# Optimization experiments

Measured on AMD Instinct MI355X. Metric: run time of the kernel, lower is better.

Reference implementation:

```python
import jax, jax.numpy as jnp
import numpy as np

B, L, D_MODEL, H = 2, 2048, 1024, 16
HD = D_MODEL // H  # head dim = 64


def setup_inputs() -> dict:
    key = jax.random.key(0)
    ks = jax.random.split(key, 11)
    s = 1.0 / np.sqrt(D_MODEL)
    inp = {
        "Q": jax.random.normal(ks[0], (B, L, D_MODEL), jnp.float32),
        "K": jax.random.normal(ks[1], (B, L, D_MODEL), jnp.float32),
        "V": jax.random.normal(ks[2], (B, L, D_MODEL), jnp.float32),
        "Wq": jax.random.normal(ks[3], (D_MODEL, D_MODEL), jnp.float32) * s,
        "bq": jnp.zeros((D_MODEL,), jnp.float32),
        "Wk": jax.random.normal(ks[4], (D_MODEL, D_MODEL), jnp.float32) * s,
        "bk": jnp.zeros((D_MODEL,), jnp.float32),
        "Wv": jax.random.normal(ks[5], (D_MODEL, D_MODEL), jnp.float32) * s,
        "bv": jnp.zeros((D_MODEL,), jnp.float32),
        "Wo": jax.random.normal(ks[6], (D_MODEL, D_MODEL), jnp.float32) * s,
        "bo": jnp.zeros((D_MODEL,), jnp.float32),
    }
    return inp


def _split_heads(x):
    # [B, L, H*D] -> [B, H, L, D]
    return x.reshape(B, L, H, HD).transpose(0, 2, 1, 3)


def reference(Q, K, V, Wq, bq, Wk, bk, Wv, bv, Wo, bo):
    q = _split_heads(Q @ Wq.T + bq)
    k = _split_heads(K @ Wk.T + bk)
    v = _split_heads(V @ Wv.T + bv)
    scale = 1.0 / jnp.sqrt(jnp.asarray(HD, q.dtype))
    # full [B, H, L, L] score matrix, as in the original bmm->softmax->bmm
    scores = jnp.einsum("bhqd,bhkd->bhqk", q, k) * scale
    attn = jax.nn.softmax(scores, axis=-1)
    o = jnp.einsum("bhqk,bhkd->bhqd", attn, v)
    o = o.transpose(0, 2, 1, 3).reshape(B, L, D_MODEL)  # concat heads
    return o @ Wo.T + bo
```

## Files before the change

### kernel.cpp

```cpp
#include <hip/hip_runtime.h>
#include <math.h>
#include <stdint.h>

typedef __bf16 bf16_t;
typedef __attribute__((ext_vector_type(8))) __bf16 bf16x8;
typedef __attribute__((ext_vector_type(4))) float f32x4;
typedef __attribute__((ext_vector_type(16))) float f32x16;
typedef __attribute__((address_space(1))) unsigned int gu32;
typedef __attribute__((address_space(3))) unsigned int lu32;

#define MFMA16(a, b, c) __builtin_amdgcn_mfma_f32_16x16x32_bf16((a), (b), (c), 0, 0, 0)
#define MFMA32(a, b, c) __builtin_amdgcn_mfma_f32_32x32x16_bf16((a), (b), (c), 0, 0, 0)

__device__ __forceinline__ void gll16(const void* g, void* l) {
    __builtin_amdgcn_global_load_lds((const gu32*)(uintptr_t)g,
                                     (lu32*)(uintptr_t)l, 16, 0, 0);
}

__device__ __forceinline__ bf16x8 ld_frag68(const bf16_t* p) {
    union { bf16x8 v; uint2 u[2]; } r;
    r.u[0] = *(const uint2*)p;
    r.u[1] = *(const uint2*)(p + 4);
    return r.v;
}

__global__ __launch_bounds__(256) void convert_all(
    const float* __restrict__ Q, const float* __restrict__ K, const float* __restrict__ V,
    const float* __restrict__ Wq, const float* __restrict__ Wk, const float* __restrict__ Wv,
    const float* __restrict__ Wo, bf16_t* __restrict__ dst) {
    size_t e0 = (size_t)blockIdx.x * 2048;
    const float* src; size_t off;
    if (e0 < 4194304)       { src = Q;  off = e0; }
    else if (e0 < 8388608)  { src = K;  off = e0 - 4194304; }
    else if (e0 < 12582912) { src = V;  off = e0 - 8388608; }
    else if (e0 < 13631488) { src = Wq; off = e0 - 12582912; }
    else if (e0 < 14680064) { src = Wk; off = e0 - 13631488; }
    else if (e0 < 15728640) { src = Wv; off = e0 - 14680064; }
    else                    { src = Wo; off = e0 - 15728640; }
#pragma unroll
    for (int p = 0; p < 2; ++p) {
        int t = p * 1024 + threadIdx.x * 4;
        float4 v = *(const float4*)(src + off + t);
        union { ushort4 u; bf16_t h[4]; } pk;
        pk.h[0] = (bf16_t)v.x; pk.h[1] = (bf16_t)v.y;
        pk.h[2] = (bf16_t)v.z; pk.h[3] = (bf16_t)v.w;
        *(ushort4*)(dst + e0 + t) = pk.u;
    }
}

__global__ __launch_bounds__(256) void qkv_gemm(
    const bf16_t* __restrict__ Qb, const bf16_t* __restrict__ Kb, const bf16_t* __restrict__ Vb,
    const bf16_t* __restrict__ Wqb, const bf16_t* __restrict__ Wkb, const bf16_t* __restrict__ Wvb,
    const float* __restrict__ bq, const float* __restrict__ bk, const float* __restrict__ bv,
    bf16_t* __restrict__ qo, bf16_t* __restrict__ ko, bf16_t* __restrict__ vT) {
    constexpr int Kdim = 1024, N = 1024;
    __shared__ __attribute__((aligned(16))) bf16_t As[128 * 64];
    __shared__ __attribute__((aligned(16))) bf16_t Bs[128 * 64];

    const int tid = threadIdx.x, wave = tid >> 6, lane = tid & 63;
    const int z = blockIdx.z;
    const bf16_t* A = (z == 0) ? Qb : (z == 1) ? Kb : Vb;
    const bf16_t* W = (z == 0) ? Wqb : (z == 1) ? Wkb : Wvb;
    const float* bias = (z == 0) ? bq : (z == 1) ? bk : bv;
    const int bm = blockIdx.y * 128, bn = blockIdx.x * 128;
    const int l16 = lane & 15, quad = lane >> 4;
    const int wm = (wave >> 1) * 64, wn = (wave & 1) * 64;
    const int grow = lane >> 3, gcol = (lane & 7) * 8;

    f32x4 acc[4][4] = {};

    for (int k0 = 0; k0 < Kdim; k0 += 64) {
#pragma unroll
        for (int j = 0; j < 4; ++j) {
            int chunk = wave * 4 + j;
            int row = chunk * 8 + grow;
            gll16(A + (size_t)(bm + row) * Kdim + k0 + gcol, As + chunk * 512);
            gll16(W + (size_t)(bn + row) * Kdim + k0 + gcol, Bs + chunk * 512);
        }
        __syncthreads();
#pragma unroll
        for (int ks = 0; ks < 64; ks += 32) {
            bf16x8 af[4], bf[4];
#pragma unroll
            for (int i = 0; i < 4; ++i)
                af[i] = *(const bf16x8*)&As[(wm + i * 16 + l16) * 64 + ks + quad * 8];
#pragma unroll
            for (int i = 0; i < 4; ++i)
                bf[i] = *(const bf16x8*)&Bs[(wn + i * 16 + l16) * 64 + ks + quad * 8];
#pragma unroll
            for (int i = 0; i < 4; ++i)
#pragma unroll
                for (int j = 0; j < 4; ++j)
                    acc[i][j] = MFMA16(af[i], bf[j], acc[i][j]);
        }
        __syncthreads();
    }

    if (z < 2) {
        bf16_t* outp = (z == 0) ? qo : ko;
        const float sc = (z == 0) ? 0.125f : 1.0f;
#pragma unroll
        for (int mi = 0; mi < 4; ++mi)
#pragma unroll
            for (int nj = 0; nj < 4; ++nj) {
                int col = bn + wn + nj * 16 + l16;
                float bv_ = bias[col];
#pragma unroll
                for (int r = 0; r < 4; ++r) {
                    int row = bm + wm + mi * 16 + quad * 4 + r;
                    outp[(size_t)row * N + col] = (bf16_t)((acc[mi][nj][r] + bv_) * sc);
                }
            }
    } else {
#pragma unroll
        for (int mi = 0; mi < 4; ++mi)
#pragma unroll
            for (int nj = 0; nj < 4; ++nj) {
                int col = bn + wn + nj * 16 + l16;
                int h = col >> 6, d = col & 63;
                float bv_ = bias[col];
                int row0 = bm + wm + mi * 16 + quad * 4;
                int bb = row0 >> 11, l = row0 & 2047;
                union { ushort4 u; bf16_t h4[4]; } pk;
#pragma unroll
                for (int r = 0; r < 4; ++r) pk.h4[r] = (bf16_t)(acc[mi][nj][r] + bv_);
                *(ushort4*)&vT[(((size_t)bb * 16 + h) * 64 + d) * 2048 + l] = pk.u;
            }
    }
}

__global__ __launch_bounds__(256) void out_gemm(const bf16_t* __restrict__ A,
                                                const bf16_t* __restrict__ W,
                                                const float* __restrict__ bias,
                                                float* __restrict__ out) {
    constexpr int Kdim = 1024, N = 1024;
    __shared__ __attribute__((aligned(16))) bf16_t As[128 * 64];
    __shared__ __attribute__((aligned(16))) bf16_t Bs[128 * 64];
    const int tid = threadIdx.x, wave = tid >> 6, lane = tid & 63;
    const int bm = blockIdx.y * 128, bn = blockIdx.x * 128;
    const int l16 = lane & 15, quad = lane >> 4;
    const int wm = (wave >> 1) * 64, wn = (wave & 1) * 64;
    const int grow = lane >> 3, gcol = (lane & 7) * 8;
    f32x4 acc[4][4] = {};

    for (int k0 = 0; k0 < Kdim; k0 += 64) {
#pragma unroll
        for (int j = 0; j < 4; ++j) {
            int chunk = wave * 4 + j;
            int row = chunk * 8 + grow;
            gll16(A + (size_t)(bm + row) * Kdim + k0 + gcol, As + chunk * 512);
            gll16(W + (size_t)(bn + row) * Kdim + k0 + gcol, Bs + chunk * 512);
        }
        __syncthreads();
#pragma unroll
        for (int ks = 0; ks < 64; ks += 32) {
            bf16x8 af[4], bf[4];
#pragma unroll
            for (int i = 0; i < 4; ++i)
                af[i] = *(const bf16x8*)&As[(wm + i * 16 + l16) * 64 + ks + quad * 8];
#pragma unroll
            for (int i = 0; i < 4; ++i)
                bf[i] = *(const bf16x8*)&Bs[(wn + i * 16 + l16) * 64 + ks + quad * 8];
#pragma unroll
            for (int i = 0; i < 4; ++i)
#pragma unroll
                for (int j = 0; j < 4; ++j)
                    acc[i][j] = MFMA16(af[i], bf[j], acc[i][j]);
        }
        __syncthreads();
    }
#pragma unroll
    for (int mi = 0; mi < 4; ++mi)
#pragma unroll
        for (int nj = 0; nj < 4; ++nj) {
            int col = bn + wn + nj * 16 + l16;
            float bv_ = bias[col];
#pragma unroll
            for (int r = 0; r < 4; ++r) {
                int row = bm + wm + mi * 16 + quad * 4 + r;
                out[(size_t)row * N + col] = acc[mi][nj][r] + bv_;
            }
        }
}

__global__ __launch_bounds__(256) void attn3(const bf16_t* __restrict__ qo,
                                             const bf16_t* __restrict__ ko,
                                             const bf16_t* __restrict__ vT,
                                             bf16_t* __restrict__ Ob) {
    constexpr int L = 2048, D = 1024, HD = 64, ST = 68;
    __shared__ __attribute__((aligned(16))) bf16_t ksm[64 * ST];
    __shared__ __attribute__((aligned(16))) bf16_t vsm[64 * ST];
    __shared__ __attribute__((aligned(16))) bf16_t psm[4][32 * ST];

    const int tid = threadIdx.x, wave = tid >> 6, lane = tid & 63;
    const int l31 = lane & 31, hi = lane >> 5;
    const int b = blockIdx.y >> 4, h = blockIdx.y & 15;
    const int q0 = blockIdx.x * 128;
    bf16_t* pw = psm[wave];

    const int rloc = tid >> 2, cg = tid & 3;
    const bf16_t* kbase = ko + ((size_t)b * L + rloc) * D + h * HD + cg * 16;
    const bf16_t* vbase = vT + (((size_t)b * 16 + h) * HD + rloc) * L + cg * 16;

    bf16x8 qf[4];
    {
        const bf16_t* qptr = qo + ((size_t)b * L + q0 + wave * 32 + l31) * D + h * HD + hi * 8;
#pragma unroll
        for (int ks = 0; ks < 4; ++ks) qf[ks] = *(const bf16x8*)(qptr + ks * 16);
    }

    f32x16 o0{}, o1{};
    float lp[16];
#pragma unroll
    for (int r = 0; r < 16; ++r) lp[r] = 0.f;

    for (int kt = 0; kt < L / 64; ++kt) {
        const size_t koff = (size_t)(kt * 64) * D;
        const int voff = kt * 64;
        uint4 ka = *(const uint4*)(kbase + koff);
        uint4 kc = *(const uint4*)(kbase + koff + 8);
        uint4 va = *(const uint4*)(vbase + voff);
        uint4 vc = *(const uint4*)(vbase + voff + 8);
        __syncthreads();
        {
            bf16_t* kd = &ksm[rloc * ST + cg * 16];
            bf16_t* vd = &vsm[rloc * ST + cg * 16];
            *(uint2*)(kd + 0)  = make_uint2(ka.x, ka.y);
            *(uint2*)(kd + 4)  = make_uint2(ka.z, ka.w);
            *(uint2*)(kd + 8)  = make_uint2(kc.x, kc.y);
            *(uint2*)(kd + 12) = make_uint2(kc.z, kc.w);
            *(uint2*)(vd + 0)  = make_uint2(va.x, va.y);
            *(uint2*)(vd + 4)  = make_uint2(va.z, va.w);
            *(uint2*)(vd + 8)  = make_uint2(vc.x, vc.y);
            *(uint2*)(vd + 12) = make_uint2(vc.z, vc.w);
        }
        __syncthreads();

        f32x16 s0{}, s1{};
#pragma unroll
        for (int ks = 0; ks < 4; ++ks) {
            bf16x8 b0 = ld_frag68(&ksm[l31 * ST + ks * 16 + hi * 8]);
            bf16x8 b1 = ld_frag68(&ksm[(32 + l31) * ST + ks * 16 + hi * 8]);
            s0 = MFMA32(qf[ks], b0, s0);
            s1 = MFMA32(qf[ks], b1, s1);
        }

#pragma unroll
        for (int r = 0; r < 16; ++r) {
            int row = (r & 3) + 8 * (r >> 2) + 4 * hi;
            float p0 = __expf(s0[r]);
            float p1 = __expf(s1[r]);
            lp[r] += p0 + p1;
            pw[row * ST + l31] = (bf16_t)p0;
            pw[row * ST + 32 + l31] = (bf16_t)p1;
        }

#pragma unroll
        for (int ks = 0; ks < 4; ++ks) {
            bf16x8 a  = ld_frag68(&pw[l31 * ST + ks * 16 + hi * 8]);
            bf16x8 b0 = ld_frag68(&vsm[l31 * ST + ks * 16 + hi * 8]);
            bf16x8 b1 = ld_frag68(&vsm[(32 + l31) * ST + ks * 16 + hi * 8]);
            o0 = MFMA32(a, b0, o0);
            o1 = MFMA32(a, b1, o1);
        }
    }

#pragma unroll
    for (int r = 0; r < 16; ++r) {
        lp[r] += __shfl_xor(lp[r], 1, 64);
        lp[r] += __shfl_xor(lp[r], 2, 64);
        lp[r] += __shfl_xor(lp[r], 4, 64);
        lp[r] += __shfl_xor(lp[r], 8, 64);
        lp[r] += __shfl_xor(lp[r], 16, 64);
    }

#pragma unroll
    for (int r = 0; r < 16; ++r) {
        int row = (r & 3) + 8 * (r >> 2) + 4 * hi;
        float inv = 1.f / lp[r];
        size_t base = ((size_t)b * L + q0 + wave * 32 + row) * D + h * HD;
        Ob[base + l31] = (bf16_t)(o0[r] * inv);
        Ob[base + 32 + l31] = (bf16_t)(o1[r] * inv);
    }
}

extern "C" void kernel_launch(void* const* d_in, const int* in_sizes, int n_in,
                              void* d_out, int out_size, void* d_ws, size_t ws_size,
                              hipStream_t stream) {
    const float* Q  = (const float*)d_in[0];
    const float* Kx = (const float*)d_in[1];
    const float* V  = (const float*)d_in[2];
    const float* Wq = (const float*)d_in[3];
    const float* bq = (const float*)d_in[4];
    const float* Wk = (const float*)d_in[5];
    const float* bk = (const float*)d_in[6];
    const float* Wv = (const float*)d_in[7];
    const float* bv = (const float*)d_in[8];
    const float* Wo = (const float*)d_in[9];
    const float* bo = (const float*)d_in[10];

    bf16_t* ws0 = (bf16_t*)d_ws;
    bf16_t* Qb  = ws0;
    bf16_t* Kb  = ws0 + 4194304;
    bf16_t* Vb  = ws0 + 8388608;
    bf16_t* Wqb = ws0 + 12582912;
    bf16_t* Wkb = ws0 + 13631488;
    bf16_t* Wvb = ws0 + 14680064;
    bf16_t* Wob = ws0 + 15728640;
    bf16_t* vT  = ws0 + 16777216;
    bf16_t* qo = (bf16_t*)d_out;
    bf16_t* ko = qo + 4194304;
    bf16_t* Ob = Qb;

    convert_all<<<8192, 256, 0, stream>>>(Q, Kx, V, Wq, Wk, Wv, Wo, ws0);
    qkv_gemm<<<dim3(8, 32, 3), 256, 0, stream>>>(Qb, Kb, Vb, Wqb, Wkb, Wvb,
                                                 bq, bk, bv, qo, ko, vT);
    attn3<<<dim3(16, 32), 256, 0, stream>>>(qo, ko, vT, Ob);
    out_gemm<<<dim3(8, 32), 256, 0, stream>>>(Ob, Wob, bo, (float*)d_out);
}
```

Baseline: 260.0 us.

## Split attention over keys, use exp2 with folded scale, shrink out-GEMM tiles

Attention is split into two key-range halves via a z grid dimension, writing unnormalized partial outputs and row sums that a new combine kernel adds and normalizes. The Q scale folds in log2(e) so exp2f replaces __expf, and K rows are permuted at store time so P can be written as packed bf16 pairs. The output GEMM uses 64-row tiles for twice as many blocks. The split and smaller tiles target low occupancy on a 512-block grid, at the cost of an extra kernel and partial-buffer traffic. The code keeps no running max in the softmax, so large scores could overflow.

```diff
diff --git a/kernel.cpp b/kernel.cpp
--- a/kernel.cpp
+++ b/kernel.cpp
@@ -3,6 +3,7 @@
 #include <stdint.h>
 
 typedef __bf16 bf16_t;
+typedef __attribute__((ext_vector_type(2))) __bf16 bf16x2;
 typedef __attribute__((ext_vector_type(8))) __bf16 bf16x8;
 typedef __attribute__((ext_vector_type(4))) float f32x4;
 typedef __attribute__((ext_vector_type(16))) float f32x16;
@@ -98,7 +99,7 @@
 
     if (z < 2) {
         bf16_t* outp = (z == 0) ? qo : ko;
-        const float sc = (z == 0) ? 0.125f : 1.0f;
+        const float sc = (z == 0) ? 0.18033688011112042f : 1.0f;
 #pragma unroll
         for (int mi = 0; mi < 4; ++mi)
 #pragma unroll
@@ -108,7 +109,12 @@
 #pragma unroll
                 for (int r = 0; r < 4; ++r) {
                     int row = bm + wm + mi * 16 + quad * 4 + r;
-                    outp[(size_t)row * N + col] = (bf16_t)((acc[mi][nj][r] + bv_) * sc);
+                    int srow = row;
+                    if (z == 1) {
+                        int w = row & 63;
+                        srow = (row & ~63) | ((w & 1) ? 32 + (w >> 1) : (w >> 1));
+                    }
+                    outp[(size_t)srow * N + col] = (bf16_t)((acc[mi][nj][r] + bv_) * sc);
                 }
             }
     } else {
@@ -134,35 +140,40 @@
                                                 const float* __restrict__ bias,
                                                 float* __restrict__ out) {
     constexpr int Kdim = 1024, N = 1024;
-    __shared__ __attribute__((aligned(16))) bf16_t As[128 * 64];
+    __shared__ __attribute__((aligned(16))) bf16_t As[64 * 64];
     __shared__ __attribute__((aligned(16))) bf16_t Bs[128 * 64];
     const int tid = threadIdx.x, wave = tid >> 6, lane = tid & 63;
-    const int bm = blockIdx.y * 128, bn = blockIdx.x * 128;
+    const int bm = blockIdx.y * 64, bn = blockIdx.x * 128;
     const int l16 = lane & 15, quad = lane >> 4;
-    const int wm = (wave >> 1) * 64, wn = (wave & 1) * 64;
+    const int wm = (wave >> 1) * 32, wn = (wave & 1) * 64;
     const int grow = lane >> 3, gcol = (lane & 7) * 8;
-    f32x4 acc[4][4] = {};
+    f32x4 acc[2][4] = {};
 
     for (int k0 = 0; k0 < Kdim; k0 += 64) {
+#pragma unroll
+        for (int j = 0; j < 2; ++j) {
+            int chunk = wave * 2 + j;
+            int row = chunk * 8 + grow;
+            gll16(A + (size_t)(bm + row) * Kdim + k0 + gcol, As + chunk * 512);
+        }
 #pragma unroll
         for (int j = 0; j < 4; ++j) {
             int chunk = wave * 4 + j;
             int row = chunk * 8 + grow;
-            gll16(A + (size_t)(bm + row) * Kdim + k0 + gcol, As + chunk * 512);
             gll16(W + (size_t)(bn + row) * Kdim + k0 + gcol, Bs + chunk * 512);
         }
         __syncthreads();
 #pragma unroll
         for (int ks = 0; ks < 64; ks += 32) {
-            bf16x8 af[4], bf[4];
-#pragma unroll
-            for (int i = 0; i < 4; ++i)
+            bf16x8 af[2], bf[4];
+#pragma unroll
+            for (int i = 0; i < 2; ++i)
                 af[i] = *(const bf16x8*)&As[(wm + i * 16 + l16) * 64 + ks + quad * 8];
 #pragma unroll
             for (int i = 0; i < 4; ++i)
                 bf[i] = *(const bf16x8*)&Bs[(wn + i * 16 + l16) * 64 + ks + quad * 8];
 #pragma unroll
-            for (int i = 0; i < 4; ++i)
+            for (int i = 0; i < 2; ++i)
 #pragma unroll
                 for (int j = 0; j < 4; ++j)
                     acc[i][j] = MFMA16(af[i], bf[j], acc[i][j]);
@@ -170,7 +181,7 @@
         __syncthreads();
     }
 #pragma unroll
-    for (int mi = 0; mi < 4; ++mi)
+    for (int mi = 0; mi < 2; ++mi)
 #pragma unroll
         for (int nj = 0; nj < 4; ++nj) {
             int col = bn + wn + nj * 16 + l16;
@@ -183,11 +194,12 @@
         }
 }
 
-__global__ __launch_bounds__(256) void attn3(const bf16_t* __restrict__ qo,
-                                             const bf16_t* __restrict__ ko,
-                                             const bf16_t* __restrict__ vT,
-                                             bf16_t* __restrict__ Ob) {
-    constexpr int L = 2048, D = 1024, HD = 64, ST = 68;
+__global__ __launch_bounds__(256, 4) void attn5(const bf16_t* __restrict__ qo,
+                                                const bf16_t* __restrict__ ko,
+                                                const bf16_t* __restrict__ vT,
+                                                bf16_t* __restrict__ Op,
+                                                float* __restrict__ lpp) {
+    constexpr int L = 2048, D = 1024, ST = 68;
     __shared__ __attribute__((aligned(16))) bf16_t ksm[64 * ST];
     __shared__ __attribute__((aligned(16))) bf16_t vsm[64 * ST];
     __shared__ __attribute__((aligned(16))) bf16_t psm[4][32 * ST];
@@ -196,15 +208,18 @@
     const int l31 = lane & 31, hi = lane >> 5;
     const int b = blockIdx.y >> 4, h = blockIdx.y & 15;
     const int q0 = blockIdx.x * 128;
+    const int split = blockIdx.z;
     bf16_t* pw = psm[wave];
+    bf16_t* Opart = Op + (size_t)split * 4194304;
+    float* lpart = lpp + split * 65536;
 
     const int rloc = tid >> 2, cg = tid & 3;
-    const bf16_t* kbase = ko + ((size_t)b * L + rloc) * D + h * HD + cg * 16;
-    const bf16_t* vbase = vT + (((size_t)b * 16 + h) * HD + rloc) * L + cg * 16;
+    const bf16_t* kbase = ko + ((size_t)b * L + rloc) * D + h * 64 + cg * 16;
+    const bf16_t* vbase = vT + (((size_t)b * 16 + h) * 64 + rloc) * L + cg * 16;
 
     bf16x8 qf[4];
     {
-        const bf16_t* qptr = qo + ((size_t)b * L + q0 + wave * 32 + l31) * D + h * HD + hi * 8;
+        const bf16_t* qptr = qo + ((size_t)b * L + q0 + wave * 32 + l31) * D + h * 64 + hi * 8;
 #pragma unroll
         for (int ks = 0; ks < 4; ++ks) qf[ks] = *(const bf16x8*)(qptr + ks * 16);
     }
@@ -214,7 +229,8 @@
 #pragma unroll
     for (int r = 0; r < 16; ++r) lp[r] = 0.f;
 
-    for (int kt = 0; kt < L / 64; ++kt) {
+    const int kt0 = split * 16, kt1 = kt0 + 16;
+    for (int kt = kt0; kt < kt1; ++kt) {
         const size_t koff = (size_t)(kt * 64) * D;
         const int voff = kt * 64;
         uint4 ka = *(const uint4*)(kbase + koff);
@@ -248,11 +264,10 @@
 #pragma unroll
         for (int r = 0; r < 16; ++r) {
             int row = (r & 3) + 8 * (r >> 2) + 4 * hi;
-            float p0 = __expf(s0[r]);
-            float p1 = __expf(s1[r]);
+            float p0 = exp2f(s0[r]);
+            float p1 = exp2f(s1[r]);
             lp[r] += p0 + p1;
-            pw[row * ST + l31] = (bf16_t)p0;
-            pw[row * ST + 32 + l31] = (bf16_t)p1;
+            *(bf16x2*)&pw[row * ST + 2 * l31] = bf16x2{(bf16_t)p0, (bf16_t)p1};
         }
 
 #pragma unroll
@@ -277,11 +292,30 @@
 #pragma unroll
     for (int r = 0; r < 16; ++r) {
         int row = (r & 3) + 8 * (r >> 2) + 4 * hi;
-        float inv = 1.f / lp[r];
-        size_t base = ((size_t)b * L + q0 + wave * 32 + row) * D + h * HD;
-        Ob[base + l31] = (bf16_t)(o0[r] * inv);
-        Ob[base + 32 + l31] = (bf16_t)(o1[r] * inv);
-    }
+        size_t base = ((size_t)b * L + q0 + wave * 32 + row) * D + h * 64;
+        Opart[base + l31] = (bf16_t)o0[r];
+        Opart[base + 32 + l31] = (bf16_t)o1[r];
+        if (l31 == 0)
+            lpart[((size_t)b * 16 + h) * 2048 + q0 + wave * 32 + row] = lp[r];
+    }
+}
+
+__global__ __launch_bounds__(256) void combine(const bf16_t* __restrict__ Op,
+                                               const float* __restrict__ lpp,
+                                               bf16_t* __restrict__ Ob) {
+    const size_t c = (size_t)blockIdx.x * 256 + threadIdx.x;
+    const int bl = (int)(c >> 7);
+    const int h = ((int)c >> 3) & 15;
+    const int bb = bl >> 11, l = bl & 2047;
+    const int li = (bb * 16 + h) * 2048 + l;
+    const float inv = 1.f / (lpp[li] + lpp[65536 + li]);
+    union { uint4 u; bf16_t h8[8]; } a, b, o;
+    a.u = *(const uint4*)(Op + c * 8);
+    b.u = *(const uint4*)(Op + 4194304 + c * 8);
+#pragma unroll
+    for (int i = 0; i < 8; ++i)
+        o.h8[i] = (bf16_t)(((float)a.h8[i] + (float)b.h8[i]) * inv);
+    *(uint4*)(Ob + c * 8) = o.u;
 }
 
 extern "C" void kernel_launch(void* const* d_in, const int* in_sizes, int n_in,
@@ -308,13 +342,16 @@
     bf16_t* Wvb = ws0 + 14680064;
     bf16_t* Wob = ws0 + 15728640;
     bf16_t* vT  = ws0 + 16777216;
+    bf16_t* Op  = Qb;
+    bf16_t* Obf = Vb;
+    float*  lpp = (float*)Wqb;
     bf16_t* qo = (bf16_t*)d_out;
     bf16_t* ko = qo + 4194304;
-    bf16_t* Ob = Qb;
 
     convert_all<<<8192, 256, 0, stream>>>(Q, Kx, V, Wq, Wk, Wv, Wo, ws0);
     qkv_gemm<<<dim3(8, 32, 3), 256, 0, stream>>>(Qb, Kb, Vb, Wqb, Wkb, Wvb,
                                                  bq, bk, bv, qo, ko, vT);
-    attn3<<<dim3(16, 32), 256, 0, stream>>>(qo, ko, vT, Ob);
-    out_gemm<<<dim3(8, 32), 256, 0, stream>>>(Ob, Wob, bo, (float*)d_out);
-}
+    attn5<<<dim3(16, 32, 2), 256, 0, stream>>>(qo, ko, vT, Op, lpp);
+    combine<<<2048, 256, 0, stream>>>(Op, lpp, Obf);
+    out_gemm<<<dim3(8, 64), 256, 0, stream>>>(Obf, Wob, bo, (float*)d_out);
+}
```

Result: faster. 254.0 us (-2.3%).
